# Kernel optimization log

Measured on AMD Instinct MI355X. Metric: run time of the kernel, lower is better.

The kernel has to match this reference:

```python
import jax, jax.numpy as jnp
import numpy as np

NEG_SLOPE = 0.2  # PyG GATConv default negative_slope


def gat_layer(x, src, dst, W, b, att_src, att_dst, heads, concat):
    """PyG-style GATConv (eval mode, self-loops already in src/dst).
    x: [N, F_in], W: [F_in, heads*hd], att_*: [heads, hd], b: [out_dim].
    """
    N = x.shape[0]
    hd = W.shape[1] // heads
    h = (x @ W).reshape(N, heads, hd)                      # [N, H, D]
    a_s = jnp.einsum('nhd,hd->nh', h, att_src)             # [N, H]
    a_d = jnp.einsum('nhd,hd->nh', h, att_dst)             # [N, H]
    e = jax.nn.leaky_relu(a_s[src] + a_d[dst], NEG_SLOPE)  # [E, H]
    # segment softmax over edges sharing a destination node
    m = jax.ops.segment_max(e, dst, num_segments=N)        # [N, H]
    m = jnp.where(jnp.isfinite(m), m, 0.0)
    ex = jnp.exp(e - m[dst])
    den = jax.ops.segment_sum(ex, dst, num_segments=N)     # [N, H]
    alpha = ex / (den[dst] + 1e-16)                        # [E, H]
    out = jax.ops.segment_sum(h[src] * alpha[:, :, None], dst, num_segments=N)  # [N,H,D]
    out = out.reshape(N, heads * hd) if concat else out.mean(axis=1)
    return out + b


def setup_inputs() -> dict:
    key = jax.random.key(0)
    ks = jax.random.split(key, 16)
    N, E, F_IN, HID, H, C = 100000, 1600000, 256, 128, 8, 6
    HD = HID // H
    s = 0.1
    return {
        'x': jax.random.normal(ks[0], (N, F_IN), jnp.float32),
        'edge_index': jax.random.randint(ks[1], (2, E), 0, N, jnp.int64),
        'W1': jax.random.normal(ks[2], (F_IN, HID), jnp.float32) * s,
        'b1': jnp.zeros((HID,), jnp.float32),
        'att_src1': jax.random.normal(ks[3], (H, HD), jnp.float32) * s,
        'att_dst1': jax.random.normal(ks[4], (H, HD), jnp.float32) * s,
        'W2': jax.random.normal(ks[5], (HID, HID), jnp.float32) * s,
        'b2': jnp.zeros((HID,), jnp.float32),
        'att_src2': jax.random.normal(ks[6], (H, HD), jnp.float32) * s,
        'att_dst2': jax.random.normal(ks[7], (H, HD), jnp.float32) * s,
        'W3': jax.random.normal(ks[8], (HID, C), jnp.float32) * s,
        'b3': jnp.zeros((C,), jnp.float32),
        'att_src3': jax.random.normal(ks[9], (1, C), jnp.float32) * s,
        'att_dst3': jax.random.normal(ks[10], (1, C), jnp.float32) * s,
    }


def reference(x, edge_index, W1, b1, att_src1, att_dst1, W2, b2, att_src2, att_dst2,
              W3, b3, att_src3, att_dst3):
    N = x.shape[0]
    loops = jnp.arange(N, dtype=edge_index.dtype)
    src = jnp.concatenate([edge_index[0], loops])  # add self-loops (PyG default)
    dst = jnp.concatenate([edge_index[1], loops])
    h = jax.nn.elu(gat_layer(x, src, dst, W1, b1, att_src1, att_dst1, 8, True))
    h = jax.nn.elu(gat_layer(h, src, dst, W2, b2, att_src2, att_dst2, 8, True))
    return gat_layer(h, src, dst, W3, b3, att_src3, att_dst3, 1, False)
```

## Files before the change

### kernel.cpp

```cpp
#include <hip/hip_runtime.h>
#include <hip/hip_bf16.h>
#include <cstdint>

typedef unsigned short u16;
typedef __attribute__((ext_vector_type(8))) short bf16x8;
typedef __attribute__((ext_vector_type(4))) float f32x4;

#define CAP 48
#define NPB 128
#define BCAP 2560
#define SA 256
#define MAXBUK 1024

__device__ __forceinline__ float b2f(u16 u){
  union { unsigned int i; float f; } v; v.i = ((unsigned int)u) << 16; return v.f;
}
__device__ __forceinline__ u16 f2b(float f){
  union { float f; unsigned int i; } v; v.f = f;
  unsigned int x = v.i;
  x += 0x7fff + ((x >> 16) & 1);
  return (u16)(x >> 16);
}
__device__ __forceinline__ float lrelu(float x){ return x > 0.f ? x : 0.2f * x; }

__global__ void k_flags(const u16* __restrict__ xr, const int* __restrict__ ei,
                        int* __restrict__ flags){
  __shared__ float smax[256];
  int t = threadIdx.x;
  float v = fabsf(b2f(xr[t * 2]));
  if (!isfinite(v)) v = 1e30f;
  smax[t] = v;
  __syncthreads();
  for (int off = 128; off > 0; off >>= 1){
    if (t < off) smax[t] = fmaxf(smax[t], smax[t + off]);
    __syncthreads();
  }
  if (t == 0){
    flags[0] = (smax[0] > 1e4f) ? 1 : 0;
    int allz = 1;
    for (int i = 1; i < 32; i += 2) if (ei[i] != 0) allz = 0;
    flags[1] = allz;
    flags[2] = 0;
    flags[3] = 0;
  }
}

#define PW_W1 0
#define PW_B1 32768
#define PW_AS1 32896
#define PW_AD1 33024
#define PW_W2 33152
#define PW_B2 49536
#define PW_AS2 49664
#define PW_AD2 49792
#define PW_W3 49920
#define PW_B3 50688
#define PW_AS3 50694
#define PW_AD3 50700
#define PW_TOTAL 50706

__global__ void k_cvt_params(const void* p0, const void* p1, const void* p2, const void* p3,
                             const void* p4, const void* p5, const void* p6, const void* p7,
                             const void* p8, const void* p9, const void* p10, const void* p11,
                             u16* __restrict__ pw, const int* __restrict__ flags){
  int i = blockIdx.x * blockDim.x + threadIdx.x;
  if (i >= PW_TOTAL) return;
  const int sizes[12] = {32768,128,128,128,16384,128,128,128,768,6,6,6};
  const void* ptrs[12] = {p0,p1,p2,p3,p4,p5,p6,p7,p8,p9,p10,p11};
  int off = 0, seg = 0, loc = 0;
  for (int s = 0; s < 12; s++){
    if (i < off + sizes[s]){ seg = s; loc = i - off; break; }
    off += sizes[s];
  }
  float v = flags[0] ? ((const float*)ptrs[seg])[loc] : b2f(((const u16*)ptrs[seg])[loc]);
  pw[i] = f2b(v);
}

__global__ void k_transpose(const u16* __restrict__ src, u16* __restrict__ dst, int R, int C){
  int i = blockIdx.x * blockDim.x + threadIdx.x;
  if (i >= R * C) return;
  int r = i / C, c = i - r * C;
  dst[(size_t)c * R + r] = src[i];
}

__device__ __forceinline__ int eread(const int* __restrict__ ei, int idx, int is64){
  return ei[is64 ? (idx << 1) : idx];
}

__global__ __launch_bounds__(256) void k_part_gemm1(const int* __restrict__ ei, int E,
                                                    unsigned* __restrict__ bbuf,
                                                    int* __restrict__ gcnt, int NBUK,
                                                    const int* __restrict__ flags,
                                                    const void* __restrict__ Xv,
                                                    const u16* __restrict__ WT,
                                                    u16* __restrict__ Ho, int N){
  if ((int)blockIdx.x < SA){
    __shared__ int hist[MAXBUK];
    __shared__ int sbase[MAXBUK];
    int tid = threadIdx.x;
    int is64 = flags[1];
    int e0 = (int)((long long)blockIdx.x * E / SA);
    int e1 = (int)((long long)((int)blockIdx.x + 1) * E / SA);
    for (int i = tid; i < NBUK; i += 256) hist[i] = 0;
    __syncthreads();
    int i = e0 + tid;
    for (; i + 7 * 256 < e1; i += 8 * 256){
      int d[8];
      #pragma unroll
      for (int u = 0; u < 8; u++) d[u] = eread(ei, E + i + u * 256, is64);
      #pragma unroll
      for (int u = 0; u < 8; u++) atomicAdd(&hist[d[u] >> 7], 1);
    }
    for (; i < e1; i += 256){
      int d = eread(ei, E + i, is64);
      atomicAdd(&hist[d >> 7], 1);
    }
    __syncthreads();
    for (int j = tid; j < NBUK; j += 256){
      sbase[j] = atomicAdd(&gcnt[j], hist[j]);
      hist[j] = 0;
    }
    __syncthreads();
    i = e0 + tid;
    for (; i + 7 * 256 < e1; i += 8 * 256){
      int s[8], d[8];
      #pragma unroll
      for (int u = 0; u < 8; u++){
        s[u] = eread(ei, i + u * 256, is64);
        d[u] = eread(ei, E + i + u * 256, is64);
      }
      #pragma unroll
      for (int u = 0; u < 8; u++){
        int b = d[u] >> 7;
        int r = sbase[b] + atomicAdd(&hist[b], 1);
        if (r < BCAP)
          bbuf[(size_t)b * BCAP + r] = ((unsigned)s[u] << 7) | (unsigned)(d[u] & (NPB - 1));
      }
    }
    for (; i < e1; i += 256){
      int s = eread(ei, i, is64);
      int d = eread(ei, E + i, is64);
      int b = d >> 7;
      int r = sbase[b] + atomicAdd(&hist[b], 1);
      if (r < BCAP)
        bbuf[(size_t)b * BCAP + r] = ((unsigned)s << 7) | (unsigned)(d & (NPB - 1));
    }
    return;
  }
  constexpr int K = 256;
  int bid = (int)blockIdx.x - SA;
  int gwave = (bid * 256 + (int)threadIdx.x) >> 6;
  int lane = threadIdx.x & 63;
  int n0 = gwave * 32;
  if (n0 >= N) return;
  int quad = lane >> 4, l15 = lane & 15;
  int r0 = n0 + l15;        if (r0 >= N) r0 = N - 1;
  int r1 = n0 + 16 + l15;   if (r1 >= N) r1 = N - 1;
  const u16* wbase = WT + (size_t)l15 * K + quad * 8;
  f32x4 acc[2][8] = {};
  if (flags[0]){
    const float* x0p = (const float*)Xv + (size_t)r0 * K + quad * 8;
    const float* x1p = (const float*)Xv + (size_t)r1 * K + quad * 8;
    for (int k0 = 0; k0 < K; k0 += 32){
      float4 v00 = *(const float4*)(x0p + k0);
      float4 v01 = *(const float4*)(x0p + k0 + 4);
      float4 v10 = *(const float4*)(x1p + k0);
      float4 v11 = *(const float4*)(x1p + k0 + 4);
      bf16x8 a0, a1;
      a0[0]=(short)f2b(v00.x); a0[1]=(short)f2b(v00.y); a0[2]=(short)f2b(v00.z); a0[3]=(short)f2b(v00.w);
      a0[4]=(short)f2b(v01.x); a0[5]=(short)f2b(v01.y); a0[6]=(short)f2b(v01.z); a0[7]=(short)f2b(v01.w);
      a1[0]=(short)f2b(v10.x); a1[1]=(short)f2b(v10.y); a1[2]=(short)f2b(v10.z); a1[3]=(short)f2b(v10.w);
      a1[4]=(short)f2b(v11.x); a1[5]=(short)f2b(v11.y); a1[6]=(short)f2b(v11.z); a1[7]=(short)f2b(v11.w);
      #pragma unroll
      for (int c = 0; c < 8; c++){
        bf16x8 b = *(const bf16x8*)(wbase + (size_t)c * 16 * K + k0);
        acc[0][c] = __builtin_amdgcn_mfma_f32_16x16x32_bf16(a0, b, acc[0][c], 0, 0, 0);
        acc[1][c] = __builtin_amdgcn_mfma_f32_16x16x32_bf16(a1, b, acc[1][c], 0, 0, 0);
      }
    }
  } else {
    const u16* x0p = (const u16*)Xv + (size_t)r0 * K + quad * 8;
    const u16* x1p = (const u16*)Xv + (size_t)r1 * K + quad * 8;
    for (int k0 = 0; k0 < K; k0 += 32){
      bf16x8 a0 = *(const bf16x8*)(x0p + k0);
      bf16x8 a1 = *(const bf16x8*)(x1p + k0);
      #pragma unroll
      for (int c = 0; c < 8; c++){
        bf16x8 b = *(const bf16x8*)(wbase + (size_t)c * 16 * K + k0);
        acc[0][c] = __builtin_amdgcn_mfma_f32_16x16x32_bf16(a0, b, acc[0][c], 0, 0, 0);
        acc[1][c] = __builtin_amdgcn_mfma_f32_16x16x32_bf16(a1, b, acc[1][c], 0, 0, 0);
      }
    }
  }
  #pragma unroll
  for (int t = 0; t < 2; t++){
    #pragma unroll
    for (int c = 0; c < 8; c++){
      #pragma unroll
      for (int r = 0; r < 4; r++){
        int row = n0 + t * 16 + quad * 4 + r;
        if (row < N) Ho[(size_t)row * 128 + c * 16 + l15] = f2b(acc[t][c][r]);
      }
    }
  }
}

__global__ __launch_bounds__(256) void k_build_att(const unsigned* __restrict__ bbuf,
                                                   const int* __restrict__ gcnt,
                                                   int* __restrict__ cnt, int* __restrict__ ebuf,
                                                   int NBUK, int N,
                                                   const u16* __restrict__ Hbuf,
                                                   const u16* __restrict__ AS,
                                                   const u16* __restrict__ AD,
                                                   float* __restrict__ as_o,
                                                   float* __restrict__ ad_o){
  if ((int)blockIdx.x < NBUK){
    __shared__ int lcnt[NPB];
    __shared__ int lrow[NPB * CAP];
    int b = blockIdx.x, tid = threadIdx.x;
    for (int i = tid; i < NPB; i += 256) lcnt[i] = 0;
    __syncthreads();
    int m = gcnt[b]; if (m > BCAP) m = BCAP;
    const unsigned* bp = bbuf + (size_t)b * BCAP;
    int i = tid;
    for (; i + 3 * 256 < m; i += 4 * 256){
      unsigned e[4];
      #pragma unroll
      for (int u = 0; u < 4; u++) e[u] = bp[i + u * 256];
      #pragma unroll
      for (int u = 0; u < 4; u++){
        int dl = e[u] & (NPB - 1);
        int p = atomicAdd(&lcnt[dl], 1);
        if (p < CAP) lrow[dl * CAP + p] = (int)(e[u] >> 7);
      }
    }
    for (; i < m; i += 256){
      unsigned e = bp[i];
      int dl = e & (NPB - 1);
      int p = atomicAdd(&lcnt[dl], 1);
      if (p < CAP) lrow[dl * CAP + p] = (int)(e >> 7);
    }
    __syncthreads();
    int n0 = b * NPB;
    int lim = N - n0; if (lim > NPB) lim = NPB;
    for (int i2 = tid; i2 < lim; i2 += 256) cnt[n0 + i2] = lcnt[i2];
    constexpr int GPN = CAP / 4;
    for (int i2 = tid; i2 < lim * GPN; i2 += 256){
      int nd = i2 / GPN, g = i2 - nd * GPN;
      int need = lcnt[nd]; if (need > CAP) need = CAP;
      if (g * 4 < need){
        int4 v = *(const int4*)&lrow[nd * CAP + g * 4];
        *(int4*)&ebuf[(size_t)(n0 + nd) * CAP + g * 4] = v;
      }
    }
    return;
  }
  int t = ((int)blockIdx.x - NBUK) * 256 + (int)threadIdx.x;
  if (t >= N * 8) return;
  int n = t >> 3, h = t & 7;
  const u16* hp = Hbuf + (size_t)n * 128 + h * 16;
  bf16x8 v0 = *(const bf16x8*)hp;
  bf16x8 v1 = *(const bf16x8*)(hp + 8);
  float s1 = 0, s2 = 0;
  #pragma unroll
  for (int d = 0; d < 8; d++){
    float a = b2f((u16)v0[d]);
    float c = b2f((u16)v1[d]);
    s1 += a * b2f(AS[h * 16 + d]) + c * b2f(AS[h * 16 + 8 + d]);
    s2 += a * b2f(AD[h * 16 + d]) + c * b2f(AD[h * 16 + 8 + d]);
  }
  as_o[t] = s1; ad_o[t] = s2;
}

template<int K>
__global__ __launch_bounds__(256) void k_gemm_mfma(const void* __restrict__ Xv,
                                                   const u16* __restrict__ WT,
                                                   u16* __restrict__ Ho, int N,
                                                   const int* __restrict__ flags){
  int gwave = (blockIdx.x * blockDim.x + threadIdx.x) >> 6;
  int lane = threadIdx.x & 63;
  int n0 = gwave * 32;
  if (n0 >= N) return;
  int quad = lane >> 4, l15 = lane & 15;
  int r0 = n0 + l15;        if (r0 >= N) r0 = N - 1;
  int r1 = n0 + 16 + l15;   if (r1 >= N) r1 = N - 1;
  const u16* wbase = WT + (size_t)l15 * K + quad * 8;
  f32x4 acc[2][8] = {};
  const u16* x0p = (const u16*)Xv + (size_t)r0 * K + quad * 8;
  const u16* x1p = (const u16*)Xv + (size_t)r1 * K + quad * 8;
  for (int k0 = 0; k0 < K; k0 += 32){
    bf16x8 a0 = *(const bf16x8*)(x0p + k0);
    bf16x8 a1 = *(const bf16x8*)(x1p + k0);
    #pragma unroll
    for (int c = 0; c < 8; c++){
      bf16x8 b = *(const bf16x8*)(wbase + (size_t)c * 16 * K + k0);
      acc[0][c] = __builtin_amdgcn_mfma_f32_16x16x32_bf16(a0, b, acc[0][c], 0, 0, 0);
      acc[1][c] = __builtin_amdgcn_mfma_f32_16x16x32_bf16(a1, b, acc[1][c], 0, 0, 0);
    }
  }
  #pragma unroll
  for (int t = 0; t < 2; t++){
    #pragma unroll
    for (int c = 0; c < 8; c++){
      #pragma unroll
      for (int r = 0; r < 4; r++){
        int row = n0 + t * 16 + quad * 4 + r;
        if (row < N) Ho[(size_t)row * 128 + c * 16 + l15] = f2b(acc[t][c][r]);
      }
    }
  }
}

__global__ __launch_bounds__(256) void k_gemm3(const u16* __restrict__ X, const u16* __restrict__ W,
                                               u16* __restrict__ Ho, int N){
  __shared__ float sW[128 * 6];
  for (int i = threadIdx.x; i < 128 * 6; i += blockDim.x) sW[i] = b2f(W[i]);
  __syncthreads();
  int n = blockIdx.x * blockDim.x + threadIdx.x;
  if (n >= N) return;
  const u16* xr = X + (size_t)n * 128;
  float acc[6] = {0, 0, 0, 0, 0, 0};
  #pragma unroll 8
  for (int k = 0; k < 128; k += 2){
    unsigned int xp = *(const unsigned int*)(xr + k);
    float x0 = b2f((u16)(xp & 0xffff));
    float x1 = b2f((u16)(xp >> 16));
    const float* w0 = sW + k * 6;
    #pragma unroll
    for (int j = 0; j < 6; j++) acc[j] += x0 * w0[j] + x1 * w0[6 + j];
  }
  u16* out = Ho + (size_t)n * 6;
  #pragma unroll
  for (int j = 0; j < 6; j++) out[j] = f2b(acc[j]);
}

template<int H, int D>
__global__ __launch_bounds__(256) void k_att(const u16* __restrict__ Hbuf,
                                             const u16* __restrict__ AS, const u16* __restrict__ AD,
                                             float* __restrict__ as_o, float* __restrict__ ad_o, int N){
  int t = blockIdx.x * blockDim.x + threadIdx.x;
  if (t >= N * H) return;
  int n = t / H, h = t - n * H;
  const u16* hp = Hbuf + (size_t)n * (H * D) + h * D;
  float s1 = 0, s2 = 0;
  if constexpr (D % 16 == 0){
    #pragma unroll
    for (int d0 = 0; d0 < D; d0 += 16){
      bf16x8 v0 = *(const bf16x8*)(hp + d0);
      bf16x8 v1 = *(const bf16x8*)(hp + d0 + 8);
      #pragma unroll
      for (int d = 0; d < 8; d++){
        float a = b2f((u16)v0[d]);
        float c = b2f((u16)v1[d]);
        s1 += a * b2f(AS[h * D + d0 + d]) + c * b2f(AS[h * D + d0 + 8 + d]);
        s2 += a * b2f(AD[h * D + d0 + d]) + c * b2f(AD[h * D + d0 + 8 + d]);
      }
    }
  } else {
    #pragma unroll
    for (int d = 0; d < D; d++){
      float v = b2f(hp[d]);
      s1 += v * b2f(AS[h * D + d]);
      s2 += v * b2f(AD[h * D + d]);
    }
  }
  as_o[t] = s1; ad_o[t] = s2;
}

__global__ __launch_bounds__(256) void k_agg8(const u16* __restrict__ Hbuf,
                                              const float* __restrict__ as,
                                              const float* __restrict__ ad,
                                              const int* __restrict__ cnt,
                                              const int* __restrict__ ebuf,
                                              const u16* __restrict__ bias,
                                              u16* __restrict__ outv, int N){
  __shared__ float wbuf[4][CAP * 8];
  __shared__ int   srow[4][CAP];
  __shared__ float dbuf[4][8];
  __shared__ float sbuf[4][8];
  int wslot = threadIdx.x >> 6;
  int lane  = threadIdx.x & 63;
  int n = (int)((blockIdx.x * blockDim.x + threadIdx.x) >> 6);
  if (n >= N) n = N - 1;
  int h = lane >> 3, jslot = lane & 7;
  int nh8 = n * 8 + h;
  float adi = ad[nh8];
  int deg = cnt[n]; if (deg > CAP) deg = CAP;
  if (lane < deg) srow[wslot][lane] = ebuf[(size_t)n * CAP + lane];
  __syncthreads();
  float wself = __expf(lrelu(as[nh8] + adi));
  {
    int r[6];
    #pragma unroll
    for (int k = 0; k < 6; k++){
      int j = jslot + 8 * k;
      r[k] = (j < deg) ? srow[wslot][j] : -1;
    }
    float w[6];
    #pragma unroll
    for (int k = 0; k < 6; k++){
      w[k] = 0.f;
      if (r[k] >= 0) w[k] = __expf(lrelu(as[r[k] * 8 + h] + adi));
    }
    float dpart = 0.f;
    #pragma unroll
    for (int k = 0; k < 6; k++){
      int j = jslot + 8 * k;
      if (j < deg){ wbuf[wslot][j * 8 + h] = w[k]; dpart += w[k]; }
    }
    dpart += __shfl_xor(dpart, 1);
    dpart += __shfl_xor(dpart, 2);
    dpart += __shfl_xor(dpart, 4);
    if (jslot == 0){ dbuf[wslot][h] = wself + dpart; sbuf[wslot][h] = wself; }
  }
  __syncthreads();
  int half = lane >> 5, l5 = lane & 31, h2 = l5 >> 2;
  float dsum = dbuf[wslot][h2];
  float wself2 = sbuf[wslot][h2];
  const u16* base = Hbuf + l5 * 4;
  float a0 = 0.f, a1 = 0.f, a2 = 0.f, a3 = 0.f;
  if (half == 0){
    uint2 q = *(const uint2*)(base + (size_t)n * 128);
    a0 = wself2 * b2f((u16)(q.x & 0xffff));
    a1 = wself2 * b2f((u16)(q.x >> 16));
    a2 = wself2 * b2f((u16)(q.y & 0xffff));
    a3 = wself2 * b2f((u16)(q.y >> 16));
  }
  const float* wrow = &wbuf[wslot][h2];
  const int* sr = srow[wslot];
  int j = half;
  for (; j + 6 < deg; j += 8){
    int s0 = sr[j], s1 = sr[j + 2], s2 = sr[j + 4], s3 = sr[j + 6];
    uint2 q0 = *(const uint2*)(base + (size_t)s0 * 128);
    uint2 q1 = *(const uint2*)(base + (size_t)s1 * 128);
    uint2 q2 = *(const uint2*)(base + (size_t)s2 * 128);
    uint2 q3 = *(const uint2*)(base + (size_t)s3 * 128);
    float w0 = wrow[j * 8],       w1 = wrow[(j + 2) * 8];
    float w2 = wrow[(j + 4) * 8], w3 = wrow[(j + 6) * 8];
    a0 += w0 * b2f((u16)(q0.x & 0xffff)) + w1 * b2f((u16)(q1.x & 0xffff))
        + w2 * b2f((u16)(q2.x & 0xffff)) + w3 * b2f((u16)(q3.x & 0xffff));
    a1 += w0 * b2f((u16)(q0.x >> 16)) + w1 * b2f((u16)(q1.x >> 16))
        + w2 * b2f((u16)(q2.x >> 16)) + w3 * b2f((u16)(q3.x >> 16));
    a2 += w0 * b2f((u16)(q0.y & 0xffff)) + w1 * b2f((u16)(q1.y & 0xffff))
        + w2 * b2f((u16)(q2.y & 0xffff)) + w3 * b2f((u16)(q3.y & 0xffff));
    a3 += w0 * b2f((u16)(q0.y >> 16)) + w1 * b2f((u16)(q1.y >> 16))
        + w2 * b2f((u16)(q2.y >> 16)) + w3 * b2f((u16)(q3.y >> 16));
  }
  for (; j < deg; j += 2){
    int s = sr[j];
    uint2 q = *(const uint2*)(base + (size_t)s * 128);
    float w = wrow[j * 8];
    a0 += w * b2f((u16)(q.x & 0xffff));
    a1 += w * b2f((u16)(q.x >> 16));
    a2 += w * b2f((u16)(q.y & 0xffff));
    a3 += w * b2f((u16)(q.y >> 16));
  }
  a0 += __shfl_xor(a0, 32);
  a1 += __shfl_xor(a1, 32);
  a2 += __shfl_xor(a2, 32);
  a3 += __shfl_xor(a3, 32);
  if (half == 0){
    float inv = 1.f / (dsum + 1e-16f);
    int jidx = l5 * 4;
    a0 = a0 * inv + b2f(bias[jidx]);
    a1 = a1 * inv + b2f(bias[jidx + 1]);
    a2 = a2 * inv + b2f(bias[jidx + 2]);
    a3 = a3 * inv + b2f(bias[jidx + 3]);
    a0 = a0 > 0.f ? a0 : expm1f(a0);
    a1 = a1 > 0.f ? a1 : expm1f(a1);
    a2 = a2 > 0.f ? a2 : expm1f(a2);
    a3 = a3 > 0.f ? a3 : expm1f(a3);
    uint2 pk;
    pk.x = (unsigned)f2b(a0) | ((unsigned)f2b(a1) << 16);
    pk.y = (unsigned)f2b(a2) | ((unsigned)f2b(a3) << 16);
    *(uint2*)(outv + (size_t)n * 128 + jidx) = pk;
  }
}

__global__ __launch_bounds__(256) void k_agg1(const u16* __restrict__ Hbuf,
                                              const float* __restrict__ as,
                                              const float* __restrict__ ad,
                                              const int* __restrict__ cnt,
                                              const int* __restrict__ ebuf,
                                              const u16* __restrict__ bias,
                                              void* __restrict__ outv,
                                              const int* __restrict__ flags, int N){
  int lane = threadIdx.x & 63;
  int n = (int)((blockIdx.x * blockDim.x + threadIdx.x) >> 6);
  if (n >= N) n = N - 1;
  int j8 = lane >> 3, c = lane & 7;
  float adi = ad[n];
  int deg = cnt[n]; if (deg > CAP) deg = CAP;
  float den = 0.f, a0 = 0.f, a1 = 0.f;
  if (j8 == 0){
    float wself = __expf(lrelu(as[n] + adi));
    den = wself;
    if (c < 3){
      unsigned q = *(const unsigned*)(Hbuf + (size_t)n * 6 + 2 * c);
      a0 = wself * b2f((u16)(q & 0xffff));
      a1 = wself * b2f((u16)(q >> 16));
    }
  }
  const int* row = ebuf + (size_t)n * CAP;
  int e = j8;
  for (; e + 8 < deg; e += 16){
    int s0 = row[e], s1 = row[e + 8];
    float v0 = as[s0], v1 = as[s1];
    unsigned q0 = 0, q1 = 0;
    if (c < 3){
      q0 = *(const unsigned*)(Hbuf + (size_t)s0 * 6 + 2 * c);
      q1 = *(const unsigned*)(Hbuf + (size_t)s1 * 6 + 2 * c);
    }
    float w0 = __expf(lrelu(v0 + adi));
    float w1 = __expf(lrelu(v1 + adi));
    den += w0 + w1;
    a0 += w0 * b2f((u16)(q0 & 0xffff)) + w1 * b2f((u16)(q1 & 0xffff));
    a1 += w0 * b2f((u16)(q0 >> 16)) + w1 * b2f((u16)(q1 >> 16));
  }
  for (; e < deg; e += 8){
    int s = row[e];
    float v = as[s];
    unsigned q = 0;
    if (c < 3) q = *(const unsigned*)(Hbuf + (size_t)s * 6 + 2 * c);
    float w = __expf(lrelu(v + adi));
    den += w;
    a0 += w * b2f((u16)(q & 0xffff));
    a1 += w * b2f((u16)(q >> 16));
  }
  #pragma unroll
  for (int m = 8; m < 64; m <<= 1){
    den += __shfl_xor(den, m);
    a0  += __shfl_xor(a0, m);
    a1  += __shfl_xor(a1, m);
  }
  if (j8 == 0 && c < 3){
    float inv = 1.f / (den + 1e-16f);
    a0 = a0 * inv + b2f(bias[2 * c]);
    a1 = a1 * inv + b2f(bias[2 * c + 1]);
    if (flags[0]){
      *(float2*)((float*)outv + (size_t)n * 6 + 2 * c) = make_float2(a0, a1);
    } else {
      unsigned pk = (unsigned)f2b(a0) | ((unsigned)f2b(a1) << 16);
      *(unsigned*)((u16*)outv + (size_t)n * 6 + 2 * c) = pk;
    }
  }
}

extern "C" void kernel_launch(void* const* d_in, const int* in_sizes, int n_in,
                              void* d_out, int out_size, void* d_ws, size_t ws_size,
                              hipStream_t stream){
  const void* x   = d_in[0];
  const int*  ei  = (const int*)d_in[1];

  const int N = in_sizes[0] / 256;
  const int E = in_sizes[1] / 2;
  const int NBUK = (N + NPB - 1) / NPB;

  char* p = (char*)d_ws;
  auto alloc = [&](size_t bytes){ void* q = (void*)p; p += (bytes + 255) & ~(size_t)255; return q; };
  int*      flags  = (int*)alloc(256);
  int*      cnt    = (int*)alloc((size_t)N * 4);
  int*      ebuf   = (int*)alloc((size_t)N * CAP * 4);
  u16*      hbuf   = (u16*)alloc((size_t)N * 128 * 2);
  float*    asb    = (float*)alloc((size_t)N * 8 * 4);
  float*    adb    = (float*)alloc((size_t)N * 8 * 4);
  u16*      x2     = (u16*)alloc((size_t)N * 128 * 2);
  u16*      x3     = (u16*)alloc((size_t)N * 128 * 2);
  u16*      pw     = (u16*)alloc((size_t)PW_TOTAL * 2);
  u16*      wt1    = (u16*)alloc((size_t)128 * 256 * 2);
  u16*      wt2    = (u16*)alloc((size_t)128 * 128 * 2);
  unsigned* bbuf   = (unsigned*)alloc((size_t)NBUK * BCAP * 4);
  int*      gcnt   = (int*)alloc((size_t)NBUK * 4);

  const int tb = 256;

  k_flags<<<1, 256, 0, stream>>>((const u16*)x, ei, flags);
  k_cvt_params<<<(PW_TOTAL + tb - 1) / tb, tb, 0, stream>>>(
      d_in[2], d_in[3], d_in[4], d_in[5], d_in[6], d_in[7],
      d_in[8], d_in[9], d_in[10], d_in[11], d_in[12], d_in[13], pw, flags);
  k_transpose<<<(32768 + tb - 1) / tb, tb, 0, stream>>>(pw + PW_W1, wt1, 256, 128);
  k_transpose<<<(16384 + tb - 1) / tb, tb, 0, stream>>>(pw + PW_W2, wt2, 128, 128);
  hipMemsetAsync(gcnt, 0, (size_t)NBUK * 4, stream);

  int gemm_blocks = (N + 127) / 128;
  int att_blocks  = (N * 8 + tb - 1) / tb;
  int agg_blocks  = (int)(((size_t)N * 64 + tb - 1) / tb);

  k_part_gemm1<<<SA + gemm_blocks, tb, 0, stream>>>(ei, E, bbuf, gcnt, NBUK, flags,
                                                    x, wt1, hbuf, N);
  k_build_att<<<NBUK + att_blocks, tb, 0, stream>>>(bbuf, gcnt, cnt, ebuf, NBUK, N,
                                                    hbuf, pw + PW_AS1, pw + PW_AD1, asb, adb);
  k_agg8<<<agg_blocks, tb, 0, stream>>>(hbuf, asb, adb, cnt, ebuf, pw + PW_B1, x2, N);

  k_gemm_mfma<128><<<gemm_blocks, tb, 0, stream>>>(x2, wt2, hbuf, N, flags + 2);
  k_att<8, 16><<<att_blocks, tb, 0, stream>>>(hbuf, pw + PW_AS2, pw + PW_AD2, asb, adb, N);
  k_agg8<<<agg_blocks, tb, 0, stream>>>(hbuf, asb, adb, cnt, ebuf, pw + PW_B2, x3, N);

  k_gemm3<<<(N + tb - 1) / tb, tb, 0, stream>>>(x3, pw + PW_W3, hbuf, N);
  k_att<1, 6><<<(N + tb - 1) / tb, tb, 0, stream>>>(hbuf, pw + PW_AS3, pw + PW_AD3, asb, adb, N);
  k_agg1<<<agg_blocks, tb, 0, stream>>>(hbuf, asb, adb, cnt, ebuf, pw + PW_B3, d_out, flags, N);
}
```

Before: 513.8 us.

## Fuse attention-score dot products into GEMM epilogues for all three layers

Computes the per-node, per-head source and destination attention scores directly from the fp32 MFMA accumulators inside each GEMM kernel, using cross-lane shuffle reductions. This removes the separate attention kernels and the re-read of the bf16 projected features. The build kernel is split out to handle only edge bucketing. Scores now come from unrounded fp32 values rather than bf16, and the shuffle epilogue adds register pressure to the GEMM kernels.

```diff
diff --git a/kernel.cpp b/kernel.cpp
--- a/kernel.cpp
+++ b/kernel.cpp
@@ -87,13 +87,60 @@
   return ei[is64 ? (idx << 1) : idx];
 }
 
+__device__ __forceinline__ void att_epilogue(const f32x4 acc[2][8], int n0, int quad, int l15,
+                                             const u16* __restrict__ AS, const u16* __restrict__ AD,
+                                             float* __restrict__ as_o, float* __restrict__ ad_o,
+                                             int N){
+  float asv[8], adv[8];
+  #pragma unroll
+  for (int c = 0; c < 8; c++){
+    asv[c] = b2f(AS[c * 16 + l15]);
+    adv[c] = b2f(AD[c * 16 + l15]);
+  }
+  #pragma unroll
+  for (int t = 0; t < 2; t++){
+    #pragma unroll
+    for (int r = 0; r < 4; r++){
+      float ps[8], pd[8];
+      #pragma unroll
+      for (int c = 0; c < 8; c++){
+        float v = acc[t][c][r];
+        ps[c] = v * asv[c];
+        pd[c] = v * adv[c];
+      }
+      #pragma unroll
+      for (int m = 1; m < 16; m <<= 1){
+        #pragma unroll
+        for (int c = 0; c < 8; c++){
+          ps[c] += __shfl_xor(ps[c], m);
+          pd[c] += __shfl_xor(pd[c], m);
+        }
+      }
+      int row = n0 + t * 16 + quad * 4 + r;
+      if (l15 < 8 && row < N){
+        float vs = ps[0], vd = pd[0];
+        #pragma unroll
+        for (int c = 1; c < 8; c++){
+          if (l15 == c){ vs = ps[c]; vd = pd[c]; }
+        }
+        as_o[row * 8 + l15] = vs;
+        ad_o[row * 8 + l15] = vd;
+      }
+    }
+  }
+}
+
 __global__ __launch_bounds__(256) void k_part_gemm1(const int* __restrict__ ei, int E,
                                                     unsigned* __restrict__ bbuf,
                                                     int* __restrict__ gcnt, int NBUK,
                                                     const int* __restrict__ flags,
                                                     const void* __restrict__ Xv,
                                                     const u16* __restrict__ WT,
-                                                    u16* __restrict__ Ho, int N){
+                                                    u16* __restrict__ Ho, int N,
+                                                    const u16* __restrict__ AS,
+                                                    const u16* __restrict__ AD,
+                                                    float* __restrict__ as_o,
+                                                    float* __restrict__ ad_o){
   if ((int)blockIdx.x < SA){
     __shared__ int hist[MAXBUK];
     __shared__ int sbase[MAXBUK];
@@ -203,80 +250,61 @@
       }
     }
   }
-}
-
-__global__ __launch_bounds__(256) void k_build_att(const unsigned* __restrict__ bbuf,
-                                                   const int* __restrict__ gcnt,
-                                                   int* __restrict__ cnt, int* __restrict__ ebuf,
-                                                   int NBUK, int N,
-                                                   const u16* __restrict__ Hbuf,
+  att_epilogue(acc, n0, quad, l15, AS, AD, as_o, ad_o, N);
+}
+
+__global__ __launch_bounds__(256) void k_build(const unsigned* __restrict__ bbuf,
+                                               const int* __restrict__ gcnt,
+                                               int* __restrict__ cnt, int* __restrict__ ebuf,
+                                               int N){
+  __shared__ int lcnt[NPB];
+  __shared__ int lrow[NPB * CAP];
+  int b = blockIdx.x, tid = threadIdx.x;
+  for (int i = tid; i < NPB; i += 256) lcnt[i] = 0;
+  __syncthreads();
+  int m = gcnt[b]; if (m > BCAP) m = BCAP;
+  const unsigned* bp = bbuf + (size_t)b * BCAP;
+  int i = tid;
+  for (; i + 3 * 256 < m; i += 4 * 256){
+    unsigned e[4];
+    #pragma unroll
+    for (int u = 0; u < 4; u++) e[u] = bp[i + u * 256];
+    #pragma unroll
+    for (int u = 0; u < 4; u++){
+      int dl = e[u] & (NPB - 1);
+      int p = atomicAdd(&lcnt[dl], 1);
+      if (p < CAP) lrow[dl * CAP + p] = (int)(e[u] >> 7);
+    }
+  }
+  for (; i < m; i += 256){
+    unsigned e = bp[i];
+    int dl = e & (NPB - 1);
+    int p = atomicAdd(&lcnt[dl], 1);
+    if (p < CAP) lrow[dl * CAP + p] = (int)(e >> 7);
+  }
+  __syncthreads();
+  int n0 = b * NPB;
+  int lim = N - n0; if (lim > NPB) lim = NPB;
+  for (int i2 = tid; i2 < lim; i2 += 256) cnt[n0 + i2] = lcnt[i2];
+  constexpr int GPN = CAP / 4;
+  for (int i2 = tid; i2 < lim * GPN; i2 += 256){
+    int nd = i2 / GPN, g = i2 - nd * GPN;
+    int need = lcnt[nd]; if (need > CAP) need = CAP;
+    if (g * 4 < need){
+      int4 v = *(const int4*)&lrow[nd * CAP + g * 4];
+      *(int4*)&ebuf[(size_t)(n0 + nd) * CAP + g * 4] = v;
+    }
+  }
+}
+
+template<int K>
+__global__ __launch_bounds__(256) void k_gemm_mfma(const void* __restrict__ Xv,
+                                                   const u16* __restrict__ WT,
+                                                   u16* __restrict__ Ho, int N,
                                                    const u16* __restrict__ AS,
                                                    const u16* __restrict__ AD,
                                                    float* __restrict__ as_o,
                                                    float* __restrict__ ad_o){
-  if ((int)blockIdx.x < NBUK){
-    __shared__ int lcnt[NPB];
-    __shared__ int lrow[NPB * CAP];
-    int b = blockIdx.x, tid = threadIdx.x;
-    for (int i = tid; i < NPB; i += 256) lcnt[i] = 0;
-    __syncthreads();
-    int m = gcnt[b]; if (m > BCAP) m = BCAP;
-    const unsigned* bp = bbuf + (size_t)b * BCAP;
-    int i = tid;
-    for (; i + 3 * 256 < m; i += 4 * 256){
-      unsigned e[4];
-      #pragma unroll
-      for (int u = 0; u < 4; u++) e[u] = bp[i + u * 256];
-      #pragma unroll
-      for (int u = 0; u < 4; u++){
-        int dl = e[u] & (NPB - 1);
-        int p = atomicAdd(&lcnt[dl], 1);
-        if (p < CAP) lrow[dl * CAP + p] = (int)(e[u] >> 7);
-      }
-    }
-    for (; i < m; i += 256){
-      unsigned e = bp[i];
-      int dl = e & (NPB - 1);
-      int p = atomicAdd(&lcnt[dl], 1);
-      if (p < CAP) lrow[dl * CAP + p] = (int)(e >> 7);
-    }
-    __syncthreads();
-    int n0 = b * NPB;
-    int lim = N - n0; if (lim > NPB) lim = NPB;
-    for (int i2 = tid; i2 < lim; i2 += 256) cnt[n0 + i2] = lcnt[i2];
-    constexpr int GPN = CAP / 4;
-    for (int i2 = tid; i2 < lim * GPN; i2 += 256){
-      int nd = i2 / GPN, g = i2 - nd * GPN;
-      int need = lcnt[nd]; if (need > CAP) need = CAP;
-      if (g * 4 < need){
-        int4 v = *(const int4*)&lrow[nd * CAP + g * 4];
-        *(int4*)&ebuf[(size_t)(n0 + nd) * CAP + g * 4] = v;
-      }
-    }
-    return;
-  }
-  int t = ((int)blockIdx.x - NBUK) * 256 + (int)threadIdx.x;
-  if (t >= N * 8) return;
-  int n = t >> 3, h = t & 7;
-  const u16* hp = Hbuf + (size_t)n * 128 + h * 16;
-  bf16x8 v0 = *(const bf16x8*)hp;
-  bf16x8 v1 = *(const bf16x8*)(hp + 8);
-  float s1 = 0, s2 = 0;
-  #pragma unroll
-  for (int d = 0; d < 8; d++){
-    float a = b2f((u16)v0[d]);
-    float c = b2f((u16)v1[d]);
-    s1 += a * b2f(AS[h * 16 + d]) + c * b2f(AS[h * 16 + 8 + d]);
-    s2 += a * b2f(AD[h * 16 + d]) + c * b2f(AD[h * 16 + 8 + d]);
-  }
-  as_o[t] = s1; ad_o[t] = s2;
-}
-
-template<int K>
-__global__ __launch_bounds__(256) void k_gemm_mfma(const void* __restrict__ Xv,
-                                                   const u16* __restrict__ WT,
-                                                   u16* __restrict__ Ho, int N,
-                                                   const int* __restrict__ flags){
   int gwave = (blockIdx.x * blockDim.x + threadIdx.x) >> 6;
   int lane = threadIdx.x & 63;
   int n0 = gwave * 32;
@@ -309,12 +337,22 @@
       }
     }
   }
+  att_epilogue(acc, n0, quad, l15, AS, AD, as_o, ad_o, N);
 }
 
 __global__ __launch_bounds__(256) void k_gemm3(const u16* __restrict__ X, const u16* __restrict__ W,
-                                               u16* __restrict__ Ho, int N){
+                                               u16* __restrict__ Ho, int N,
+                                               const u16* __restrict__ AS3,
+                                               const u16* __restrict__ AD3,
+                                               float* __restrict__ as_o,
+                                               float* __restrict__ ad_o){
   __shared__ float sW[128 * 6];
+  __shared__ float sA[6], sD[6];
   for (int i = threadIdx.x; i < 128 * 6; i += blockDim.x) sW[i] = b2f(W[i]);
+  if (threadIdx.x < 6){
+    sA[threadIdx.x] = b2f(AS3[threadIdx.x]);
+    sD[threadIdx.x] = b2f(AD3[threadIdx.x]);
+  }
   __syncthreads();
   int n = blockIdx.x * blockDim.x + threadIdx.x;
   if (n >= N) return;
@@ -330,41 +368,15 @@
     for (int j = 0; j < 6; j++) acc[j] += x0 * w0[j] + x1 * w0[6 + j];
   }
   u16* out = Ho + (size_t)n * 6;
+  float s1 = 0.f, s2 = 0.f;
   #pragma unroll
-  for (int j = 0; j < 6; j++) out[j] = f2b(acc[j]);
-}
-
-template<int H, int D>
-__global__ __launch_bounds__(256) void k_att(const u16* __restrict__ Hbuf,
-                                             const u16* __restrict__ AS, const u16* __restrict__ AD,
-                                             float* __restrict__ as_o, float* __restrict__ ad_o, int N){
-  int t = blockIdx.x * blockDim.x + threadIdx.x;
-  if (t >= N * H) return;
-  int n = t / H, h = t - n * H;
-  const u16* hp = Hbuf + (size_t)n * (H * D) + h * D;
-  float s1 = 0, s2 = 0;
-  if constexpr (D % 16 == 0){
-    #pragma unroll
-    for (int d0 = 0; d0 < D; d0 += 16){
-      bf16x8 v0 = *(const bf16x8*)(hp + d0);
-      bf16x8 v1 = *(const bf16x8*)(hp + d0 + 8);
-      #pragma unroll
-      for (int d = 0; d < 8; d++){
-        float a = b2f((u16)v0[d]);
-        float c = b2f((u16)v1[d]);
-        s1 += a * b2f(AS[h * D + d0 + d]) + c * b2f(AS[h * D + d0 + 8 + d]);
-        s2 += a * b2f(AD[h * D + d0 + d]) + c * b2f(AD[h * D + d0 + 8 + d]);
-      }
-    }
-  } else {
-    #pragma unroll
-    for (int d = 0; d < D; d++){
-      float v = b2f(hp[d]);
-      s1 += v * b2f(AS[h * D + d]);
-      s2 += v * b2f(AD[h * D + d]);
-    }
-  }
-  as_o[t] = s1; ad_o[t] = s2;
+  for (int j = 0; j < 6; j++){
+    out[j] = f2b(acc[j]);
+    s1 += acc[j] * sA[j];
+    s2 += acc[j] * sD[j];
+  }
+  as_o[n] = s1;
+  ad_o[n] = s2;
 }
 
 __global__ __launch_bounds__(256) void k_agg8(const u16* __restrict__ Hbuf,
@@ -583,20 +595,19 @@
   hipMemsetAsync(gcnt, 0, (size_t)NBUK * 4, stream);
 
   int gemm_blocks = (N + 127) / 128;
-  int att_blocks  = (N * 8 + tb - 1) / tb;
   int agg_blocks  = (int)(((size_t)N * 64 + tb - 1) / tb);
 
   k_part_gemm1<<<SA + gemm_blocks, tb, 0, stream>>>(ei, E, bbuf, gcnt, NBUK, flags,
-                                                    x, wt1, hbuf, N);
-  k_build_att<<<NBUK + att_blocks, tb, 0, stream>>>(bbuf, gcnt, cnt, ebuf, NBUK, N,
-                                                    hbuf, pw + PW_AS1, pw + PW_AD1, asb, adb);
+                                                    x, wt1, hbuf, N,
+                                                    pw + PW_AS1, pw + PW_AD1, asb, adb);
+  k_build<<<NBUK, tb, 0, stream>>>(bbuf, gcnt, cnt, ebuf, N);
   k_agg8<<<agg_blocks, tb, 0, stream>>>(hbuf, asb, adb, cnt, ebuf, pw + PW_B1, x2, N);
 
-  k_gemm_mfma<128><<<gemm_blocks, tb, 0, stream>>>(x2, wt2, hbuf, N, flags + 2);
-  k_att<8, 16><<<att_blocks, tb, 0, stream>>>(hbuf, pw + PW_AS2, pw + PW_AD2, asb, adb, N);
+  k_gemm_mfma<128><<<gemm_blocks, tb, 0, stream>>>(x2, wt2, hbuf, N,
+                                                   pw + PW_AS2, pw + PW_AD2, asb, adb);
   k_agg8<<<agg_blocks, tb, 0, stream>>>(hbuf, asb, adb, cnt, ebuf, pw + PW_B2, x3, N);
 
-  k_gemm3<<<(N + tb - 1) / tb, tb, 0, stream>>>(x3, pw + PW_W3, hbuf, N);
-  k_att<1, 6><<<(N + tb - 1) / tb, tb, 0, stream>>>(hbuf, pw + PW_AS3, pw + PW_AD3, asb, adb, N);
+  k_gemm3<<<(N + tb - 1) / tb, tb, 0, stream>>>(x3, pw + PW_W3, hbuf, N,
+                                                pw + PW_AS3, pw + PW_AD3, asb, adb);
   k_agg1<<<agg_blocks, tb, 0, stream>>>(hbuf, asb, adb, cnt, ebuf, pw + PW_B3, d_out, flags, N);
 }
```

Result: slower. 530.2 us (+3.2%).
